# Kernel optimization log

Measured on AMD Instinct MI355X. Metric: run time of the kernel, lower is better.

The kernel has to match this reference:

```python
import jax, jax.numpy as jnp
import numpy as np

B, T, H, K = 64, 512, 768, 11
START_ID, END_ID = 9, 10  # tag_to_ix['<CLS>'], tag_to_ix['<SEP>']
NEG = -10000.0


def setup_inputs() -> dict:
    key = jax.random.key(0)
    k1, k2, k3, k4 = jax.random.split(key, 4)
    embeds = jax.random.normal(k1, (B, T, H), dtype=jnp.float32)
    W_fc = jax.random.normal(k2, (K, H), dtype=jnp.float32) * 0.02
    b_fc = jax.random.normal(k3, (K,), dtype=jnp.float32) * 0.02
    transitions = jax.random.normal(k4, (K, K), dtype=jnp.float32)
    # __init__ masking: no transition out of anything into START row, none into END col
    transitions = transitions.at[START_ID, :].set(NEG)
    transitions = transitions.at[:, END_ID].set(NEG)
    return {"embeds": embeds, "W_fc": W_fc, "b_fc": b_fc, "transitions": transitions}


def reference(embeds, W_fc, b_fc, transitions):
    # fc projection: feats[b,t,k] (PLM_crf path: encoder output -> Linear)
    feats = jnp.einsum('bth,kh->btk', embeds, W_fc) + b_fc  # [B,T,K]
    Bv, Tv, Kv = feats.shape

    # Viterbi: log_delta init -10000 except start tag; NOTE the original never
    # adds feats[:, 0] (loop starts at t=1), so we faithfully skip it too.
    log_delta0 = jnp.full((Bv, Kv), NEG, dtype=feats.dtype).at[:, START_ID].set(0.0)

    def step(log_delta, feat_t):
        # transitions[i, j]: score of moving from prev tag j to tag i
        scores = transitions[None, :, :] + log_delta[:, None, :]  # [B,K,K]
        psi_t = jnp.argmax(scores, axis=-1)                       # [B,K] best prev tag
        log_delta_new = jnp.max(scores, axis=-1) + feat_t         # [B,K]
        return log_delta_new, psi_t

    feats_seq = jnp.swapaxes(feats[:, 1:], 0, 1)                  # [T-1,B,K]
    log_delta, psi = jax.lax.scan(step, log_delta0, feats_seq)    # psi: [T-1,B,K]

    score = jnp.max(log_delta, axis=-1)                           # [B]
    last_tag = jnp.argmax(log_delta, axis=-1)                     # [B]

    # Backtrack: path[t] = psi[t+1][path[t+1]] for t = T-2 .. 0
    def back(next_tag, psi_t):
        tag = jnp.take_along_axis(psi_t, next_tag[:, None], axis=-1)[:, 0]
        return tag, tag

    _, path_rest = jax.lax.scan(back, last_tag, psi, reverse=True)  # [T-1,B]
    path = jnp.concatenate([jnp.swapaxes(path_rest, 0, 1), last_tag[:, None]], axis=1)  # [B,T]
    return score, path
```

## Files before the change

kernel.cpp:

```cpp
#include <hip/hip_runtime.h>

#define BB 64
#define TT 512
#define HH 768
#define KK 11
#define START_ID 9
#define NEGV -10000.0f
#define TT4 (TT + 4)

typedef float vf2 __attribute__((ext_vector_type(2)));

template <int CTRL>
__device__ __forceinline__ float dpp_add(float x) {
    int yi = __builtin_amdgcn_update_dpp(0, __float_as_int(x), CTRL, 0xF, 0xF, false);
    return x + __int_as_float(yi);
}

__device__ __forceinline__ float wave_sum_to_lane63(float x) {
    x = dpp_add<0x111>(x);
    x = dpp_add<0x112>(x);
    x = dpp_add<0x114>(x);
    x = dpp_add<0x118>(x);
    x = dpp_add<0x142>(x);
    x = dpp_add<0x143>(x);
    return x;
}

__device__ __forceinline__ float rlane(float v, int l) {
    return __int_as_float(__builtin_amdgcn_readlane(__float_as_int(v), l));
}

__global__ __launch_bounds__(256) void fc_kernel(const float* __restrict__ embeds,
                                                 const float* __restrict__ W,
                                                 const float* __restrict__ bias,
                                                 float* __restrict__ feats) {
    __shared__ __align__(16) float w_lds[KK * HH];

    const int tid = threadIdx.x;
    const int lane = tid & 63;

    {
        const float4* src = reinterpret_cast<const float4*>(W);
        float4* dst = reinterpret_cast<float4*>(w_lds);
#pragma unroll
        for (int i = 0; i < 9; ++i) {
            int idx = tid + i * 256;
            if (idx < KK * HH / 4) dst[idx] = src[idx];
        }
    }

    float bk[KK];
#pragma unroll
    for (int k = 0; k < KK; ++k) bk[k] = bias[k];

    __syncthreads();

    const int wave_id = (blockIdx.x * blockDim.x + tid) >> 6;
    const int base = wave_id * 8;
    const int lo = lane * 4;

    const float* ea = embeds + (size_t)base * HH;
    const float* eb = ea + HH;
    float4 a0 = *reinterpret_cast<const float4*>(ea + 0   + lo);
    float4 a1 = *reinterpret_cast<const float4*>(ea + 256 + lo);
    float4 a2 = *reinterpret_cast<const float4*>(ea + 512 + lo);
    float4 b0 = *reinterpret_cast<const float4*>(eb + 0   + lo);
    float4 b1 = *reinterpret_cast<const float4*>(eb + 256 + lo);
    float4 b2 = *reinterpret_cast<const float4*>(eb + 512 + lo);

#pragma unroll 1
    for (int rr = 0; rr < 8; rr += 2) {
        const int nrr = (rr + 2) & 7;
        const float* na = embeds + (size_t)(base + nrr) * HH;
        const float* nb = na + HH;
        float4 na0 = *reinterpret_cast<const float4*>(na + 0   + lo);
        float4 na1 = *reinterpret_cast<const float4*>(na + 256 + lo);
        float4 na2 = *reinterpret_cast<const float4*>(na + 512 + lo);
        float4 nb0 = *reinterpret_cast<const float4*>(nb + 0   + lo);
        float4 nb1 = *reinterpret_cast<const float4*>(nb + 256 + lo);
        float4 nb2 = *reinterpret_cast<const float4*>(nb + 512 + lo);

        vf2 va[6] = {{a0.x, a0.y}, {a0.z, a0.w}, {a1.x, a1.y},
                     {a1.z, a1.w}, {a2.x, a2.y}, {a2.z, a2.w}};
        vf2 vb[6] = {{b0.x, b0.y}, {b0.z, b0.w}, {b1.x, b1.y},
                     {b1.z, b1.w}, {b2.x, b2.y}, {b2.z, b2.w}};

        float4 w0 = *reinterpret_cast<const float4*>(w_lds + 0 + lo);
        float4 w1 = *reinterpret_cast<const float4*>(w_lds + 256 + lo);
        float4 w2 = *reinterpret_cast<const float4*>(w_lds + 512 + lo);

        float rA[KK], rB[KK];
#pragma unroll
        for (int k = 0; k < KK; ++k) {
            const int nk = (k == KK - 1) ? 0 : k + 1;
            float4 nw0 = *reinterpret_cast<const float4*>(w_lds + nk * HH + 0 + lo);
            float4 nw1 = *reinterpret_cast<const float4*>(w_lds + nk * HH + 256 + lo);
            float4 nw2 = *reinterpret_cast<const float4*>(w_lds + nk * HH + 512 + lo);

            vf2 wv[6] = {{w0.x, w0.y}, {w0.z, w0.w},
                         {w1.x, w1.y}, {w1.z, w1.w},
                         {w2.x, w2.y}, {w2.z, w2.w}};
            vf2 sA = va[0] * wv[0];
            vf2 sB = vb[0] * wv[0];
#pragma unroll
            for (int r = 1; r < 6; ++r) { sA += va[r] * wv[r]; sB += vb[r] * wv[r]; }
            rA[k] = wave_sum_to_lane63(sA.x + sA.y);
            rB[k] = wave_sum_to_lane63(sB.x + sB.y);

            w0 = nw0; w1 = nw1; w2 = nw2;
        }

        if (lane == 63) {
            float* oA = feats + (size_t)(base + rr) * KK;
#pragma unroll
            for (int k = 0; k < KK; ++k) oA[k] = rA[k] + bk[k];
#pragma unroll
            for (int k = 0; k < KK; ++k) oA[KK + k] = rB[k] + bk[k];
        }

        a0 = na0; a1 = na1; a2 = na2;
        b0 = nb0; b1 = nb1; b2 = nb2;
    }
}

__global__ __launch_bounds__(256) void viterbi_kernel(const float* __restrict__ feats,
                                                      const float* __restrict__ trans,
                                                      float* __restrict__ out) {
    __shared__ __align__(16) float featsT[KK * TT4];
    __shared__ __align__(16) float dh[(TT - 1) * 12 + 16];
    __shared__ int psi_lds[(TT - 1) * KK];
    __shared__ float tr_lds[KK * KK];
    __shared__ int comp[15 * KK];
    __shared__ int bt[16];
    __shared__ int sh_last;

    const int tid = threadIdx.x;
    const int b = blockIdx.x;

    {
        const float4* src = reinterpret_cast<const float4*>(feats + (size_t)b * TT * KK);
        for (int idx4 = tid; idx4 < TT * KK / 4; idx4 += 256) {
            float4 v = src[idx4];
            const int e = idx4 * 4;
#pragma unroll
            for (int u = 0; u < 4; ++u) {
                int t = (e + u) / KK;
                int k = (e + u) - t * KK;
                if (t > 0) featsT[k * TT4 + (t - 1)] = (&v.x)[u];
            }
        }
        if (tid < KK * KK) tr_lds[tid] = trans[tid];
    }
    __syncthreads();

    if (tid < 64) {
        const int i = tid;
        float tr[KK];
#pragma unroll
        for (int j = 0; j < KK; ++j) tr[j] = (i < KK) ? tr_lds[i * KK + j] : NEGV;

        float delta = (i == START_ID) ? 0.0f : NEGV;

        auto vstep = [&](float fcur, float& hs) {
            hs = delta;
            float dj[KK];
#pragma unroll
            for (int j = 0; j < KK; ++j) dj[j] = rlane(delta, j);
            float s[KK];
#pragma unroll
            for (int j = 0; j < KK; ++j) s[j] = tr[j] + dj[j];
            float t0 = fmaxf(fmaxf(s[0], s[1]), s[2]);
            float t1 = fmaxf(fmaxf(s[3], s[4]), s[5]);
            float t2 = fmaxf(fmaxf(s[6], s[7]), s[8]);
            float t3 = fmaxf(s[9], s[10]);
            float best = fmaxf(fmaxf(fmaxf(t0, t1), t2), t3);
            delta = best + fcur;
        };

        const int ci = (i < KK) ? i : 0;
        const float* frow = featsT + ci * TT4;
        float* dwbase = dh + i;

        float h0, h1, h2, h3, h4, h5, h6, h7;
        float h8, h9, h10, h11, h12, h13, h14, h15;

        float4 A0 = *reinterpret_cast<const float4*>(frow + 0);
        float4 A1 = *reinterpret_cast<const float4*>(frow + 4);
        float4 A2 = *reinterpret_cast<const float4*>(frow + 8);
        float4 A3 = *reinterpret_cast<const float4*>(frow + 12);

#pragma unroll 1
        for (int c = 0; c < 31; ++c) {
            const float* nf = frow + (c + 1) * 16;
            float4 B0 = *reinterpret_cast<const float4*>(nf + 0);
            float4 B1 = *reinterpret_cast<const float4*>(nf + 4);
            float4 B2 = *reinterpret_cast<const float4*>(nf + 8);
            float4 B3 = *reinterpret_cast<const float4*>(nf + 12);

            vstep(A0.x, h0);  vstep(A0.y, h1);  vstep(A0.z, h2);  vstep(A0.w, h3);
            vstep(A1.x, h4);  vstep(A1.y, h5);  vstep(A1.z, h6);  vstep(A1.w, h7);
            vstep(A2.x, h8);  vstep(A2.y, h9);  vstep(A2.z, h10); vstep(A2.w, h11);
            vstep(A3.x, h12); vstep(A3.y, h13); vstep(A3.z, h14); vstep(A3.w, h15);

            if (i < KK) {
                float* dw = dwbase + c * 192;
                dw[0]   = h0;  dw[12]  = h1;  dw[24]  = h2;  dw[36]  = h3;
                dw[48]  = h4;  dw[60]  = h5;  dw[72]  = h6;  dw[84]  = h7;
                dw[96]  = h8;  dw[108] = h9;  dw[120] = h10; dw[132] = h11;
                dw[144] = h12; dw[156] = h13; dw[168] = h14; dw[180] = h15;
            }

            A0 = B0; A1 = B1; A2 = B2; A3 = B3;
        }
        vstep(A0.x, h0);  vstep(A0.y, h1);  vstep(A0.z, h2);  vstep(A0.w, h3);
        vstep(A1.x, h4);  vstep(A1.y, h5);  vstep(A1.z, h6);  vstep(A1.w, h7);
        vstep(A2.x, h8);  vstep(A2.y, h9);  vstep(A2.z, h10); vstep(A2.w, h11);
        vstep(A3.x, h12); vstep(A3.y, h13); vstep(A3.z, h14);
        if (i < KK) {
            float* dw = dwbase + 31 * 192;
            dw[0]   = h0;  dw[12]  = h1;  dw[24]  = h2;  dw[36]  = h3;
            dw[48]  = h4;  dw[60]  = h5;  dw[72]  = h6;  dw[84]  = h7;
            dw[96]  = h8;  dw[108] = h9;  dw[120] = h10; dw[132] = h11;
            dw[144] = h12; dw[156] = h13; dw[168] = h14;
        }

        float dfin[KK];
#pragma unroll
        for (int j = 0; j < KK; ++j) dfin[j] = rlane(delta, j);
        float best = dfin[0];
        int last = 0;
#pragma unroll
        for (int j = 1; j < KK; ++j) {
            bool c = dfin[j] > best;
            best = c ? dfin[j] : best;
            last = c ? j : last;
        }
        if (tid == 0) {
            out[b] = best;
            out[BB + (size_t)b * TT + (TT - 1)] = (float)last;
            sh_last = last;
        }
    }
    __syncthreads();

    {
        const int i = tid & 15;
        const int sg = tid >> 4;
        if (i < KK) {
            float tri[KK];
#pragma unroll
            for (int j = 0; j < KK; ++j) tri[j] = tr_lds[i * KK + j];
            for (int s = sg; s < TT - 1; s += 16) {
                const float4* dr = reinterpret_cast<const float4*>(dh + s * 12);
                float4 a = dr[0], c4 = dr[1], d4 = dr[2];
                float sc[KK] = {tri[0] + a.x,  tri[1] + a.y,  tri[2] + a.z,  tri[3] + a.w,
                                tri[4] + c4.x, tri[5] + c4.y, tri[6] + c4.z, tri[7] + c4.w,
                                tri[8] + d4.x, tri[9] + d4.y, tri[10] + d4.z};
                float bv = sc[0];
                int bj = 0;
#pragma unroll
                for (int j = 1; j < KK; ++j) {
                    bool c = sc[j] > bv;
                    bv = c ? sc[j] : bv;
                    bj = c ? j : bj;
                }
                psi_lds[s * KK + i] = bj;
            }
        }
    }
    __syncthreads();

    {
        const int c = tid >> 4;
        const int i = tid & 15;
        if (c < 15 && i < KK) {
            int cur = i;
            for (int s = c * 32 + 31; s >= c * 32; --s) cur = psi_lds[s * KK + cur];
            comp[c * KK + i] = cur;
        } else if (c == 15 && i == 0) {
            int cur = sh_last;
            float* po = out + BB + (size_t)b * TT;
            for (int s = TT - 2; s >= 480; --s) {
                cur = psi_lds[s * KK + cur];
                po[s] = (float)cur;
            }
            bt[15] = cur;
        }
    }
    __syncthreads();

    if (tid == 0) {
        for (int c = 14; c >= 1; --c) bt[c] = comp[c * KK + bt[c + 1]];
    }
    __syncthreads();

    if (tid < 15) {
        const int c = tid;
        int cur = bt[c + 1];
        float* po = out + BB + (size_t)b * TT;
        for (int s = c * 32 + 31; s >= c * 32; --s) {
            cur = psi_lds[s * KK + cur];
            po[s] = (float)cur;
        }
    }
}

extern "C" void kernel_launch(void* const* d_in, const int* in_sizes, int n_in,
                              void* d_out, int out_size, void* d_ws, size_t ws_size,
                              hipStream_t stream) {
    const float* embeds = (const float*)d_in[0];
    const float* W_fc   = (const float*)d_in[1];
    const float* b_fc   = (const float*)d_in[2];
    const float* trans  = (const float*)d_in[3];
    float* out = (float*)d_out;
    float* feats = (float*)d_ws;

    fc_kernel<<<1024, 256, 0, stream>>>(embeds, W_fc, b_fc, feats);
    viterbi_kernel<<<BB, 256, 0, stream>>>(feats, trans, out);
}
```

Before: 195.8 us.

## Split Viterbi max over lane quads using bpermute and DPP reductions

Each tag now uses four lanes instead of one. Each lane gathers three previous deltas via ds_bpermute and takes a partial max, then the quad reduces with two DPP max steps. This replaces eleven serial readlane broadcasts plus a long max chain per step. It adds LDS-latency permutes on the serial recurrence path and pads the feature rows with -inf for the unused tags.

```diff
diff --git a/kernel.cpp b/kernel.cpp
--- a/kernel.cpp
+++ b/kernel.cpp
@@ -7,8 +7,11 @@
 #define START_ID 9
 #define NEGV -10000.0f
 #define TT4 (TT + 4)
+#define NROWS 16
 
 typedef float vf2 __attribute__((ext_vector_type(2)));
+
+__device__ __forceinline__ float ninf() { return __int_as_float(0xff800000); }
 
 template <int CTRL>
 __device__ __forceinline__ float dpp_add(float x) {
@@ -28,6 +31,12 @@
 
 __device__ __forceinline__ float rlane(float v, int l) {
     return __int_as_float(__builtin_amdgcn_readlane(__float_as_int(v), l));
+}
+
+template <int PAT>
+__device__ __forceinline__ float quad_fmax(float x) {
+    int yi = __builtin_amdgcn_update_dpp(0, __float_as_int(x), PAT, 0xF, 0xF, false);
+    return fmaxf(x, __int_as_float(yi));
 }
 
 __global__ __launch_bounds__(256) void fc_kernel(const float* __restrict__ embeds,
@@ -126,7 +135,7 @@
 __global__ __launch_bounds__(256) void viterbi_kernel(const float* __restrict__ feats,
                                                       const float* __restrict__ trans,
                                                       float* __restrict__ out) {
-    __shared__ __align__(16) float featsT[KK * TT4];
+    __shared__ __align__(16) float featsT[NROWS * TT4];
     __shared__ __align__(16) float dh[(TT - 1) * 12 + 16];
     __shared__ int psi_lds[(TT - 1) * KK];
     __shared__ float tr_lds[KK * KK];
@@ -149,36 +158,40 @@
                 if (t > 0) featsT[k * TT4 + (t - 1)] = (&v.x)[u];
             }
         }
+        for (int x = tid; x < (NROWS - KK) * TT4; x += 256)
+            featsT[KK * TT4 + x] = ninf();
         if (tid < KK * KK) tr_lds[tid] = trans[tid];
     }
     __syncthreads();
 
     if (tid < 64) {
-        const int i = tid;
-        float tr[KK];
-#pragma unroll
-        for (int j = 0; j < KK; ++j) tr[j] = (i < KK) ? tr_lds[i * KK + j] : NEGV;
-
-        float delta = (i == START_ID) ? 0.0f : NEGV;
+        const int i = tid >> 2;
+        const int q = tid & 3;
+
+        float trq0, trq1, trq2;
+        {
+            const int j0 = 3 * q, j1 = 3 * q + 1, j2 = 3 * q + 2;
+            trq0 = (i < KK && j0 < KK) ? tr_lds[i * KK + j0] : 0.0f;
+            trq1 = (i < KK && j1 < KK) ? tr_lds[i * KK + j1] : 0.0f;
+            trq2 = (i < KK && j2 < KK) ? tr_lds[i * KK + j2] : 0.0f;
+        }
+        const int a0 = 48 * q, a1 = 48 * q + 16, a2 = 48 * q + 32;
+
+        float delta = (i == START_ID) ? 0.0f : ((i < KK) ? NEGV : ninf());
 
         auto vstep = [&](float fcur, float& hs) {
             hs = delta;
-            float dj[KK];
-#pragma unroll
-            for (int j = 0; j < KK; ++j) dj[j] = rlane(delta, j);
-            float s[KK];
-#pragma unroll
-            for (int j = 0; j < KK; ++j) s[j] = tr[j] + dj[j];
-            float t0 = fmaxf(fmaxf(s[0], s[1]), s[2]);
-            float t1 = fmaxf(fmaxf(s[3], s[4]), s[5]);
-            float t2 = fmaxf(fmaxf(s[6], s[7]), s[8]);
-            float t3 = fmaxf(s[9], s[10]);
-            float best = fmaxf(fmaxf(fmaxf(t0, t1), t2), t3);
-            delta = best + fcur;
+            const int di = __float_as_int(delta);
+            float d0 = __int_as_float(__builtin_amdgcn_ds_bpermute(a0, di));
+            float d1 = __int_as_float(__builtin_amdgcn_ds_bpermute(a1, di));
+            float d2 = __int_as_float(__builtin_amdgcn_ds_bpermute(a2, di));
+            float m = fmaxf(fmaxf(trq0 + d0, trq1 + d1), trq2 + d2);
+            m = quad_fmax<0xB1>(m);
+            m = quad_fmax<0x4E>(m);
+            delta = m + fcur;
         };
 
-        const int ci = (i < KK) ? i : 0;
-        const float* frow = featsT + ci * TT4;
+        const float* frow = featsT + i * TT4;
         float* dwbase = dh + i;
 
         float h0, h1, h2, h3, h4, h5, h6, h7;
@@ -202,7 +215,7 @@
             vstep(A2.x, h8);  vstep(A2.y, h9);  vstep(A2.z, h10); vstep(A2.w, h11);
             vstep(A3.x, h12); vstep(A3.y, h13); vstep(A3.z, h14); vstep(A3.w, h15);
 
-            if (i < KK) {
+            if (q == 0 && i < KK) {
                 float* dw = dwbase + c * 192;
                 dw[0]   = h0;  dw[12]  = h1;  dw[24]  = h2;  dw[36]  = h3;
                 dw[48]  = h4;  dw[60]  = h5;  dw[72]  = h6;  dw[84]  = h7;
@@ -216,7 +229,7 @@
         vstep(A1.x, h4);  vstep(A1.y, h5);  vstep(A1.z, h6);  vstep(A1.w, h7);
         vstep(A2.x, h8);  vstep(A2.y, h9);  vstep(A2.z, h10); vstep(A2.w, h11);
         vstep(A3.x, h12); vstep(A3.y, h13); vstep(A3.z, h14);
-        if (i < KK) {
+        if (q == 0 && i < KK) {
             float* dw = dwbase + 31 * 192;
             dw[0]   = h0;  dw[12]  = h1;  dw[24]  = h2;  dw[36]  = h3;
             dw[48]  = h4;  dw[60]  = h5;  dw[72]  = h6;  dw[84]  = h7;
@@ -226,7 +239,7 @@
 
         float dfin[KK];
 #pragma unroll
-        for (int j = 0; j < KK; ++j) dfin[j] = rlane(delta, j);
+        for (int j = 0; j < KK; ++j) dfin[j] = rlane(delta, 4 * j);
         float best = dfin[0];
         int last = 0;
 #pragma unroll
```

After: 200.6 us. 1.02x slower.
